# Kernel tuning notes

Measured on AMD Instinct MI355X. Metric: run time of the kernel, lower is better.

The kernel has to match this reference:

```python
import jax, jax.numpy as jnp
import numpy as np

N, IN, HID, H, OUT, G = 2048, 128, 128, 4, 10, 8
NEG_SLOPE = 0.2
THRESHOLD = 0.0


def setup_inputs() -> dict:
    key = jax.random.key(0)
    ks = jax.random.split(key, 18)
    s = 0.05
    return {
        "x": jax.random.normal(ks[0], (N, IN), jnp.float32),
        "attn_tensor": jax.random.normal(ks[1], (12, N, N), jnp.float32),
        "batch_idx": jnp.sort(jax.random.randint(ks[2], (N,), 0, G)),
        "conv_w": jax.random.normal(ks[3], (12,), jnp.float32) * s,
        "conv_b": jnp.zeros((), jnp.float32),
        "W1": jax.random.normal(ks[4], (IN, H * HID), jnp.float32) * s,
        "att_src1": jax.random.normal(ks[5], (H, HID), jnp.float32) * s,
        "att_dst1": jax.random.normal(ks[6], (H, HID), jnp.float32) * s,
        "att_edge1": jax.random.normal(ks[7], (H, HID), jnp.float32) * s,
        "We1": jax.random.normal(ks[8], (H * HID,), jnp.float32) * s,
        "b1": jnp.zeros((H * HID,), jnp.float32),
        "W2": jax.random.normal(ks[9], (H * HID, HID), jnp.float32) * s,
        "att_src2": jax.random.normal(ks[10], (1, HID), jnp.float32) * s,
        "att_dst2": jax.random.normal(ks[11], (1, HID), jnp.float32) * s,
        "att_edge2": jax.random.normal(ks[12], (1, HID), jnp.float32) * s,
        "We2": jax.random.normal(ks[13], (HID,), jnp.float32) * s,
        "b2": jnp.zeros((HID,), jnp.float32),
        "fc_w": jax.random.normal(ks[14], (HID, OUT), jnp.float32) * s,
        "fc_b": jnp.zeros((OUT,), jnp.float32),
    }


def gat_layer(x, adj, eattr, W, a_src, a_dst, a_edge, We, b, heads, out_ch):
    n = x.shape[0]
    h = (x @ W).reshape(n, heads, out_ch)            # [N,H,C]
    s_src = jnp.einsum('nhc,hc->nh', h, a_src)       # alpha contribution of source node
    s_dst = jnp.einsum('nhc,hc->nh', h, a_dst)       # alpha contribution of target node
    c_e = jnp.einsum('hc,hc->h', a_edge, We.reshape(heads, out_ch))  # scalar edge coeff per head
    # logits[s,t,h] for message s -> t (edge (s,t) means agg_mat[s,t] > thr)
    logits = s_src[:, None, :] + s_dst[None, :, :] + eattr[:, :, None] * c_e[None, None, :]
    logits = jnp.where(logits >= 0, logits, NEG_SLOPE * logits)  # leaky_relu(0.2)
    logits = jnp.where(adj[:, :, None], logits, -1e9)
    alpha = jax.nn.softmax(logits, axis=0)           # segment softmax over sources per target
    out = jnp.einsum('sth,shc->thc', alpha, h).reshape(n, heads * out_ch)
    return out + b


def reference(x, attn_tensor, batch_idx, conv_w, conv_b,
              W1, att_src1, att_dst1, att_edge1, We1, b1,
              W2, att_src2, att_dst2, att_edge2, We2, b2,
              fc_w, fc_b):
    # 1x1 conv over 12 attention channels -> dense [N,N] aggregated matrix
    agg = jnp.einsum('c,cst->st', conv_w, attn_tensor) + conv_b
    eye = jnp.eye(N, dtype=bool)
    mask_off = (agg > THRESHOLD) & (~eye)            # PyG GATConv removes then re-adds self loops
    # self-loop edge_attr = mean of incoming edge attrs per target (fill_value='mean')
    cnt = mask_off.sum(axis=0)
    mean_attr = jnp.where(mask_off, agg, 0.0).sum(axis=0) / jnp.maximum(cnt, 1)
    eattr = jnp.where(mask_off, agg, 0.0) + jnp.diag(mean_attr)
    adj = mask_off | eye

    h = gat_layer(x, adj, eattr, W1, att_src1, att_dst1, att_edge1, We1, b1, H, HID)
    h = jax.nn.relu(h)
    h = gat_layer(h, adj, eattr, W2, att_src2, att_dst2, att_edge2, We2, b2, 1, HID)

    sums = jax.ops.segment_sum(h, batch_idx, num_segments=G)
    counts = jax.ops.segment_sum(jnp.ones((N,), h.dtype), batch_idx, num_segments=G)
    pooled = sums / jnp.maximum(counts, 1.0)[:, None]  # global_mean_pool
    return jax.nn.log_softmax(pooled @ fc_w + fc_b, axis=1)
```

## Files before the change

### kernel.cpp

```cpp
#include <hip/hip_runtime.h>
#include <hip/hip_bf16.h>
#include <math.h>

#define NN 2048
#define NEG_SLOPE 0.2f

typedef __attribute__((ext_vector_type(8))) short bf16x8;
typedef __attribute__((ext_vector_type(4))) float f32x4;

static __device__ inline short f2bf(float x) {
  union { float f; unsigned u; } v;
  v.f = x;
  unsigned r = v.u + 0x7fffu + ((v.u >> 16) & 1u);
  return (short)(r >> 16);
}

static __device__ inline float bf2f(short b) {
  union { unsigned u; float f; } v;
  v.u = ((unsigned)(unsigned short)b) << 16;
  return v.f;
}

__global__ __launch_bounds__(256) void k_pre(
    const float* __restrict__ attn, const float* __restrict__ conv_w,
    const float* __restrict__ conv_b, const float* __restrict__ x,
    const float* __restrict__ W1, const float* __restrict__ W2,
    const float* __restrict__ asrc1, const float* __restrict__ adst1,
    const float* __restrict__ ae1, const float* __restrict__ We1,
    const float* __restrict__ ae2, const float* __restrict__ We2,
    __hip_bfloat16* __restrict__ aggTb, float* __restrict__ ssum_part,
    float* __restrict__ scnt_part, __hip_bfloat16* __restrict__ hTsw1,
    float* __restrict__ sspart1, float* __restrict__ sdpart1,
    __hip_bfloat16* __restrict__ w2t, float* __restrict__ ce) {
  const int b = blockIdx.x;
  const int tid = threadIdx.x;
  __shared__ __align__(16) char smem[34816];
  if (b < 512) {
    typedef short w1row[136];
    w1row* w1s = (w1row*)smem;
    const int mb = b >> 2, cblk = b & 3;
    const int m0 = mb * 16;
    for (int e = tid; e < 128 * 32; e += 256) {
      int k = e >> 5, cq = (e & 31) * 4;
      f32x4 v = *(const f32x4*)(W1 + (size_t)k * 512 + cblk * 128 + cq);
#pragma unroll
      for (int j = 0; j < 4; ++j) w1s[cq + j][k] = f2bf(v[j]);
    }
    __syncthreads();
    const int wv = tid >> 6;
    const int lane = tid & 63, row = lane & 15, kg = lane >> 4;
    const int nb = cblk * 4 + wv;
    const int n0l = wv * 32;
    const float* axrow = x + (size_t)(m0 + row) * 128 + kg * 8;
    f32x4 acc[2];
#pragma unroll
    for (int f = 0; f < 2; ++f) acc[f] = (f32x4){0.f, 0.f, 0.f, 0.f};
#pragma unroll
    for (int ks = 0; ks < 4; ++ks) {
      f32x4 xa = *(const f32x4*)(axrow + ks * 32);
      f32x4 xb = *(const f32x4*)(axrow + ks * 32 + 4);
      bf16x8 Af = {f2bf(xa[0]), f2bf(xa[1]), f2bf(xa[2]), f2bf(xa[3]),
                   f2bf(xb[0]), f2bf(xb[1]), f2bf(xb[2]), f2bf(xb[3])};
#pragma unroll
      for (int f = 0; f < 2; ++f) {
        bf16x8 Bf = *(const bf16x8*)&w1s[n0l + f * 16 + row][kg * 8 + ks * 32];
        acc[f] =
            __builtin_amdgcn_mfma_f32_16x16x32_bf16(Af, Bf, acc[f], 0, 0, 0);
      }
    }
    const int h = nb >> 2;
    float as[2], ad[2];
#pragma unroll
    for (int f = 0; f < 2; ++f) {
      int ch = (n0l + f * 16 + row) & 127;
      as[f] = asrc1[h * 128 + ch];
      ad[f] = adst1[h * 128 + ch];
    }
    float ps[4] = {0.f, 0.f, 0.f, 0.f}, pd[4] = {0.f, 0.f, 0.f, 0.f};
#pragma unroll
    for (int f = 0; f < 2; ++f)
#pragma unroll
      for (int r = 0; r < 4; ++r) {
        ps[r] += acc[f][r] * as[f];
        pd[r] += acc[f][r] * ad[f];
      }
#pragma unroll
    for (int m = 1; m < 16; m <<= 1) {
#pragma unroll
      for (int r = 0; r < 4; ++r) {
        ps[r] += __shfl_xor(ps[r], m);
        pd[r] += __shfl_xor(pd[r], m);
      }
    }
    if (row == 0) {
#pragma unroll
      for (int r = 0; r < 4; ++r) {
        int node = m0 + kg * 4 + r;
        sspart1[nb * NN + node] = ps[r];
        sdpart1[nb * NN + node] = pd[r];
      }
    }
#pragma unroll
    for (int f = 0; f < 2; ++f) {
      const int cbi = nb * 2 + f;
      short4 ct;
      ct.x = f2bf(acc[f][0]); ct.y = f2bf(acc[f][1]);
      ct.z = f2bf(acc[f][2]); ct.w = f2bf(acc[f][3]);
      size_t a4 =
          (size_t)cbi * (NN * 16) +
          (size_t)(((m0 >> 3) + (kg >> 1)) * 128 + row * 8 + (kg & 1) * 4);
      *(short4*)((short*)hTsw1 + a4) = ct;
    }
  } else if (b < 1536) {
    typedef float trow[68];
    trow* tile = (trow*)smem;
    const int b2 = b - 512;
    const int t0 = (b2 & 31) * 64;
    const int s0 = (b2 >> 5) * 64;
    const int sl = tid >> 4;
    const int t4 = (tid & 15) * 4;
    float w[12];
#pragma unroll
    for (int c = 0; c < 12; ++c) w[c] = conv_w[c];
    const float cb = conv_b[0];
    f32x4 acc[4];
#pragma unroll
    for (int k = 0; k < 4; ++k) acc[k] = (f32x4){cb, cb, cb, cb};
    for (int c = 0; c < 12; ++c) {
      const float* base =
          attn + (size_t)c * NN * NN + (size_t)(s0 + sl) * NN + t0 + t4;
#pragma unroll
      for (int k = 0; k < 4; ++k)
        acc[k] += w[c] * *(const f32x4*)(base + (size_t)k * 16 * NN);
    }
#pragma unroll
    for (int k = 0; k < 4; ++k) *(f32x4*)&tile[sl + 16 * k][t4] = acc[k];
    __syncthreads();
    const int tl = tid >> 2;
    const int sq = (tid & 3) * 16;
    const int tglob = t0 + tl;
    float psum = 0.f, pcnt = 0.f;
    short bb[16];
#pragma unroll
    for (int g = 0; g < 4; ++g) {
      f32x4 v = {tile[sq + 4 * g][tl], tile[sq + 4 * g + 1][tl],
                 tile[sq + 4 * g + 2][tl], tile[sq + 4 * g + 3][tl]};
#pragma unroll
      for (int j = 0; j < 4; ++j) {
        bb[4 * g + j] = f2bf(v[j]);
        int sglob = s0 + sq + 4 * g + j;
        bool m = (v[j] > 0.f) && (sglob != tglob);
        psum += m ? v[j] : 0.f;
        pcnt += m ? 1.f : 0.f;
      }
    }
    {
      short* orow = (short*)aggTb + (size_t)tglob * NN + s0 + sq;
      bf16x8 lo = {bb[0], bb[1], bb[2], bb[3], bb[4], bb[5], bb[6], bb[7]};
      bf16x8 hi = {bb[8], bb[9], bb[10], bb[11], bb[12], bb[13], bb[14], bb[15]};
      *(bf16x8*)orow = lo;
      *(bf16x8*)(orow + 8) = hi;
    }
    psum += __shfl_down(psum, 1); psum += __shfl_down(psum, 2);
    pcnt += __shfl_down(pcnt, 1); pcnt += __shfl_down(pcnt, 2);
    if ((tid & 3) == 0) {
      ssum_part[(b2 >> 5) * NN + tglob] = psum;
      scnt_part[(b2 >> 5) * NN + tglob] = pcnt;
    }
  } else if (b < 1568) {
#pragma unroll
    for (int k = 0; k < 8; ++k) {
      int o = (b - 1536) * 2048 + k * 256 + tid;
      ((short*)w2t)[o] = f2bf(W2[(o & 511) * 128 + (o >> 9)]);
    }
  } else {
    const int lane = tid & 63;
    const int wv = tid >> 6;
    float q1 = ae1[wv * 128 + lane] * We1[wv * 128 + lane] +
               ae1[wv * 128 + 64 + lane] * We1[wv * 128 + 64 + lane];
    for (int off = 32; off; off >>= 1) q1 += __shfl_down(q1, off);
    if (lane == 0) ce[wv] = q1;
    float q2 = ae2[lane] * We2[lane] + ae2[64 + lane] * We2[64 + lane];
    for (int off = 32; off; off >>= 1) q2 += __shfl_down(q2, off);
    if (tid == 0) ce[4] = q2;
  }
}

__global__ __launch_bounds__(256) void k_attn1(
    const __hip_bfloat16* __restrict__ aggTb,
    const __hip_bfloat16* __restrict__ hTsw1,
    const float* __restrict__ sspart1, const float* __restrict__ sdpart1,
    const float* __restrict__ ssum_part, const float* __restrict__ scnt_part,
    const float* __restrict__ ce_all, const float* __restrict__ b1,
    __hip_bfloat16* __restrict__ feat1b) {
  const int tid = threadIdx.x;
  const int t0 = (int)(blockIdx.x >> 2) * 16;
  const int h = (int)(blockIdx.x & 3u);
  __shared__ float ss_sh[2048];
  __shared__ float red[4][16][128];
  __shared__ float den_sh[4][16];
  __shared__ float mp_sh[2][16][16];
  __shared__ float ma_sh[16];
  for (int i = tid; i < 2048; i += 256)
    ss_sh[i] = sspart1[(4 * h + 0) * NN + i] + sspart1[(4 * h + 1) * NN + i] +
               sspart1[(4 * h + 2) * NN + i] + sspart1[(4 * h + 3) * NN + i];
  {
    int r = tid & 15, q2 = tid >> 4;
    float s_ = ssum_part[(size_t)(2 * q2) * NN + t0 + r] +
               ssum_part[(size_t)(2 * q2 + 1) * NN + t0 + r];
    float c_ = scnt_part[(size_t)(2 * q2) * NN + t0 + r] +
               scnt_part[(size_t)(2 * q2 + 1) * NN + t0 + r];
    mp_sh[0][q2][r] = s_;
    mp_sh[1][q2][r] = c_;
  }
  __syncthreads();
  if (tid < 16) {
    float s_ = 0.f, c_ = 0.f;
#pragma unroll
    for (int q = 0; q < 16; ++q) { s_ += mp_sh[0][q][tid]; c_ += mp_sh[1][q][tid]; }
    ma_sh[tid] = s_ / fmaxf(c_, 1.f);
  }
  __syncthreads();
  const int lane = tid & 63, w = tid >> 6, row = lane & 15, kg = lane >> 4;
  const int sbeg = w * 512;
  const int tRow = t0 + row;
  const float ma_t = ma_sh[row];
  const float ce = ce_all[h];
  const float sd_t = sdpart1[(4 * h + 0) * NN + tRow] +
                     sdpart1[(4 * h + 1) * NN + tRow] +
                     sdpart1[(4 * h + 2) * NN + tRow] +
                     sdpart1[(4 * h + 3) * NN + tRow];
  const short* arowb = (const short*)aggTb + (size_t)tRow * NN;
  const float* ssh = ss_sh + sbeg;
  const __hip_bfloat16* bbase =
      hTsw1 + (size_t)(h * 8) * (NN * 16) + kg * 128 + row * 8;
  f32x4 acc[8];
#pragma unroll
  for (int f = 0; f < 8; ++f) acc[f] = (f32x4){0.f, 0.f, 0.f, 0.f};
  float dpart = 0.f;
  for (int s0 = sbeg; s0 < sbeg + 512; s0 += 32) {
    const int sk = s0 + kg * 8;
    bf16x8 araw = *(const bf16x8*)(arowb + sk);
    f32x4 sv0 = *(const f32x4*)(ssh + (sk - sbeg));
    f32x4 sv1 = *(const f32x4*)(ssh + (sk - sbeg) + 4);
    float sv[8] = {sv0[0], sv0[1], sv0[2], sv0[3],
                   sv1[0], sv1[1], sv1[2], sv1[3]};
    short pb[8];
#pragma unroll
    for (int j = 0; j < 8; ++j) {
      const int s = sk + j;
      const float a = bf2f(araw[j]);
      const bool diag = (s == tRow);
      const float ev = diag ? ma_t : a;
      const bool adj = diag || (a > 0.f);
      float l = sv[j] + sd_t + ev * ce;
      l = fmaxf(l, NEG_SLOPE * l);
      const float p = adj ? __expf(l) : 0.f;
      dpart += p;
      pb[j] = f2bf(p);
    }
    bf16x8 A = {pb[0], pb[1], pb[2], pb[3], pb[4], pb[5], pb[6], pb[7]};
    const __hip_bfloat16* bp = bbase + (size_t)s0 * 16;
#pragma unroll
    for (int f = 0; f < 8; ++f) {
      bf16x8 B = *(const bf16x8*)(bp + (size_t)f * (NN * 16));
      acc[f] = __builtin_amdgcn_mfma_f32_16x16x32_bf16(A, B, acc[f], 0, 0, 0);
    }
  }
  dpart += __shfl_xor(dpart, 16);
  dpart += __shfl_xor(dpart, 32);
  __syncthreads();
#pragma unroll
  for (int f = 0; f < 8; ++f)
#pragma unroll
    for (int r = 0; r < 4; ++r) red[w][kg * 4 + r][f * 16 + row] = acc[f][r];
  if (lane < 16) den_sh[w][lane] = dpart;
  __syncthreads();
#pragma unroll
  for (int i = 0; i < 8; ++i) {
    int idx = i * 256 + tid;
    int t = idx >> 7, c = idx & 127;
    float nsum = red[0][t][c] + red[1][t][c] + red[2][t][c] + red[3][t][c];
    float dsum = den_sh[0][t] + den_sh[1][t] + den_sh[2][t] + den_sh[3][t];
    float v = nsum / dsum + b1[h * 128 + c];
    feat1b[(size_t)(t0 + t) * 512 + h * 128 + c] =
        __float2bfloat16(v > 0.f ? v : 0.f);
  }
}

__global__ __launch_bounds__(256) void k_gemm2(
    const __hip_bfloat16* __restrict__ feat1b,
    const __hip_bfloat16* __restrict__ w2t, const float* __restrict__ asrc2,
    const float* __restrict__ adst2, __hip_bfloat16* __restrict__ hTsw2,
    float* __restrict__ ssrc2, float* __restrict__ sdst2) {
  const int tid = threadIdx.x;
  const int wv = tid >> 6;
  const int w = (int)blockIdx.x * 4 + wv;
  const int lane = tid & 63, row = lane & 15, kg = lane >> 4;
  const int mb = w >> 2, nb = w & 3;
  const int m0 = mb * 16, n0 = nb * 32;
  __shared__ float sred[2][4][16];
  const __hip_bfloat16* arow = feat1b + (size_t)(m0 + row) * 512 + kg * 8;
  f32x4 acc[2];
#pragma unroll
  for (int f = 0; f < 2; ++f) acc[f] = (f32x4){0.f, 0.f, 0.f, 0.f};
#pragma unroll
  for (int ks = 0; ks < 16; ++ks) {
    bf16x8 Af = *(const bf16x8*)(arow + ks * 32);
#pragma unroll
    for (int f = 0; f < 2; ++f) {
      bf16x8 Bf = *(const bf16x8*)(w2t + (size_t)(n0 + f * 16 + row) * 512 +
                                   kg * 8 + ks * 32);
      acc[f] = __builtin_amdgcn_mfma_f32_16x16x32_bf16(Af, Bf, acc[f], 0, 0, 0);
    }
  }
  float as[2], ad[2];
#pragma unroll
  for (int f = 0; f < 2; ++f) {
    int ch = (n0 + f * 16 + row) & 127;
    as[f] = asrc2[ch];
    ad[f] = adst2[ch];
  }
  float ps[4] = {0.f, 0.f, 0.f, 0.f}, pd[4] = {0.f, 0.f, 0.f, 0.f};
#pragma unroll
  for (int f = 0; f < 2; ++f)
#pragma unroll
    for (int r = 0; r < 4; ++r) {
      ps[r] += acc[f][r] * as[f];
      pd[r] += acc[f][r] * ad[f];
    }
#pragma unroll
  for (int m = 1; m < 16; m <<= 1) {
#pragma unroll
    for (int r = 0; r < 4; ++r) {
      ps[r] += __shfl_xor(ps[r], m);
      pd[r] += __shfl_xor(pd[r], m);
    }
  }
  if (row == 0) {
#pragma unroll
    for (int r = 0; r < 4; ++r) {
      sred[0][wv][kg * 4 + r] = ps[r];
      sred[1][wv][kg * 4 + r] = pd[r];
    }
  }
  __syncthreads();
  if (tid < 16) {
    float s = sred[0][0][tid] + sred[0][1][tid] + sred[0][2][tid] +
              sred[0][3][tid];
    float d = sred[1][0][tid] + sred[1][1][tid] + sred[1][2][tid] +
              sred[1][3][tid];
    ssrc2[(int)blockIdx.x * 16 + tid] = s;
    sdst2[(int)blockIdx.x * 16 + tid] = d;
  }
#pragma unroll
  for (int f = 0; f < 2; ++f) {
    const int cbi = nb * 2 + f;
    short4 ct;
    ct.x = f2bf(acc[f][0]); ct.y = f2bf(acc[f][1]);
    ct.z = f2bf(acc[f][2]); ct.w = f2bf(acc[f][3]);
    size_t a4 = (size_t)cbi * (NN * 16) +
                (size_t)(((m0 >> 3) + (kg >> 1)) * 128 + row * 8 + (kg & 1) * 4);
    *(short4*)((short*)hTsw2 + a4) = ct;
  }
}

__global__ __launch_bounds__(256) void k_attn2(
    const __hip_bfloat16* __restrict__ aggTb,
    const __hip_bfloat16* __restrict__ hTsw2,
    const float* __restrict__ ssrc2, const float* __restrict__ sdst2,
    const float* __restrict__ ssum_part, const float* __restrict__ scnt_part,
    const float* __restrict__ ce_all, const float* __restrict__ b2,
    float* __restrict__ feat2) {
  const int tid = threadIdx.x;
  const int t0 = (int)(blockIdx.x >> 1) * 16;
  const int chalf = (int)(blockIdx.x & 1u);
  __shared__ float ss_sh[2048];
  __shared__ float red[4][16][64];
  __shared__ float den_sh[4][16];
  __shared__ float mp_sh[2][16][16];
  __shared__ float ma_sh[16];
  for (int i = tid; i < 2048; i += 256) ss_sh[i] = ssrc2[i];
  {
    int r = tid & 15, q2 = tid >> 4;
    float s_ = ssum_part[(size_t)(2 * q2) * NN + t0 + r] +
               ssum_part[(size_t)(2 * q2 + 1) * NN + t0 + r];
    float c_ = scnt_part[(size_t)(2 * q2) * NN + t0 + r] +
               scnt_part[(size_t)(2 * q2 + 1) * NN + t0 + r];
    mp_sh[0][q2][r] = s_;
    mp_sh[1][q2][r] = c_;
  }
  __syncthreads();
  if (tid < 16) {
    float s_ = 0.f, c_ = 0.f;
#pragma unroll
    for (int q = 0; q < 16; ++q) { s_ += mp_sh[0][q][tid]; c_ += mp_sh[1][q][tid]; }
    ma_sh[tid] = s_ / fmaxf(c_, 1.f);
  }
  __syncthreads();
  const int lane = tid & 63, w = tid >> 6, row = lane & 15, kg = lane >> 4;
  const int sbeg = w * 512;
  const int tRow = t0 + row;
  const float ma_t = ma_sh[row];
  const float ce = ce_all[4];
  const float sd_t = sdst2[tRow];
  const short* arowb = (const short*)aggTb + (size_t)tRow * NN;
  const float* ssh = ss_sh + sbeg;
  const __hip_bfloat16* bbase =
      hTsw2 + (size_t)(chalf * 4) * (NN * 16) + kg * 128 + row * 8;
  f32x4 acc[4];
#pragma unroll
  for (int f = 0; f < 4; ++f) acc[f] = (f32x4){0.f, 0.f, 0.f, 0.f};
  float dpart = 0.f;
  for (int s0 = sbeg; s0 < sbeg + 512; s0 += 32) {
    const int sk = s0 + kg * 8;
    bf16x8 araw = *(const bf16x8*)(arowb + sk);
    f32x4 sv0 = *(const f32x4*)(ssh + (sk - sbeg));
    f32x4 sv1 = *(const f32x4*)(ssh + (sk - sbeg) + 4);
    float sv[8] = {sv0[0], sv0[1], sv0[2], sv0[3],
                   sv1[0], sv1[1], sv1[2], sv1[3]};
    short pb[8];
#pragma unroll
    for (int j = 0; j < 8; ++j) {
      const int s = sk + j;
      const float a = bf2f(araw[j]);
      const bool diag = (s == tRow);
      const float ev = diag ? ma_t : a;
      const bool adj = diag || (a > 0.f);
      float l = sv[j] + sd_t + ev * ce;
      l = fmaxf(l, NEG_SLOPE * l);
      const float p = adj ? __expf(l) : 0.f;
      dpart += p;
      pb[j] = f2bf(p);
    }
    bf16x8 A = {pb[0], pb[1], pb[2], pb[3], pb[4], pb[5], pb[6], pb[7]};
    const __hip_bfloat16* bp = bbase + (size_t)s0 * 16;
#pragma unroll
    for (int f = 0; f < 4; ++f) {
      bf16x8 B = *(const bf16x8*)(bp + (size_t)f * (NN * 16));
      acc[f] = __builtin_amdgcn_mfma_f32_16x16x32_bf16(A, B, acc[f], 0, 0, 0);
    }
  }
  dpart += __shfl_xor(dpart, 16);
  dpart += __shfl_xor(dpart, 32);
  __syncthreads();
#pragma unroll
  for (int f = 0; f < 4; ++f)
#pragma unroll
    for (int r = 0; r < 4; ++r) red[w][kg * 4 + r][f * 16 + row] = acc[f][r];
  if (lane < 16) den_sh[w][lane] = dpart;
  __syncthreads();
#pragma unroll
  for (int i = 0; i < 4; ++i) {
    int idx = i * 256 + tid;
    int t = idx >> 6, c = idx & 63;
    float nsum = red[0][t][c] + red[1][t][c] + red[2][t][c] + red[3][t][c];
    float dsum = den_sh[0][t] + den_sh[1][t] + den_sh[2][t] + den_sh[3][t];
    feat2[(size_t)(t0 + t) * 128 + chalf * 64 + c] =
        nsum / dsum + b2[chalf * 64 + c];
  }
}

__global__ __launch_bounds__(256) void k_poolhead(
    const float* __restrict__ feat, const int* __restrict__ bidx,
    const float* __restrict__ fcw, const float* __restrict__ fcb,
    float* __restrict__ out) {
  const int g = blockIdx.x;
  const int tid = threadIdx.x;
  __shared__ int lo[2];
  __shared__ float ps2[256];
  __shared__ float lsh[10];
  if (tid == 0) { lo[0] = NN; lo[1] = NN; }
  __syncthreads();
  for (int n = tid; n < NN; n += 256) {
    int b = bidx[n];
    int bprev = (n == 0) ? -1 : bidx[n - 1];
    if (b >= g && bprev < g) atomicMin(&lo[0], n);
    if (b >= g + 1 && bprev < g + 1) atomicMin(&lo[1], n);
  }
  __syncthreads();
  int s = lo[0], e = lo[1];
  const int c = tid & 127, half = tid >> 7;
  float sum = 0.f;
  for (int n = s + half; n < e; n += 2) sum += feat[(size_t)n * 128 + c];
  ps2[tid] = sum;
  __syncthreads();
  if (tid < 128) {
    float cntf = (float)((e - s) > 1 ? (e - s) : 1);
    ps2[tid] = (ps2[tid] + ps2[tid + 128]) / cntf;
  }
  __syncthreads();
  if (tid < 10) {
    float v = fcb[tid];
    for (int ch = 0; ch < 128; ++ch) v += ps2[ch] * fcw[ch * 10 + tid];
    lsh[tid] = v;
  }
  __syncthreads();
  if (tid < 10) {
    float m = -1e30f;
    for (int i = 0; i < 10; ++i) m = fmaxf(m, lsh[i]);
    float den = 0.f;
    for (int i = 0; i < 10; ++i) den += expf(lsh[i] - m);
    out[g * 10 + tid] = lsh[tid] - m - logf(den);
  }
}

extern "C" void kernel_launch(void* const* d_in, const int* in_sizes, int n_in,
                              void* d_out, int out_size, void* d_ws,
                              size_t ws_size, hipStream_t stream) {
  (void)in_sizes; (void)n_in; (void)out_size; (void)ws_size;
  const float* x      = (const float*)d_in[0];
  const float* attn   = (const float*)d_in[1];
  const int*   bidx   = (const int*)d_in[2];
  const float* conv_w = (const float*)d_in[3];
  const float* conv_b = (const float*)d_in[4];
  const float* W1     = (const float*)d_in[5];
  const float* asrc1  = (const float*)d_in[6];
  const float* adst1  = (const float*)d_in[7];
  const float* aedge1 = (const float*)d_in[8];
  const float* We1    = (const float*)d_in[9];
  const float* b1     = (const float*)d_in[10];
  const float* W2     = (const float*)d_in[11];
  const float* asrc2  = (const float*)d_in[12];
  const float* adst2  = (const float*)d_in[13];
  const float* aedge2 = (const float*)d_in[14];
  const float* We2    = (const float*)d_in[15];
  const float* b2     = (const float*)d_in[16];
  const float* fcw    = (const float*)d_in[17];
  const float* fcb    = (const float*)d_in[18];

  float* ws = (float*)d_ws;
  __hip_bfloat16* aggTb = (__hip_bfloat16*)ws;
  float* feat2     = ws + 2097152;
  float* ssum_part = feat2 + 262144;
  float* scnt_part = ssum_part + 65536;
  float* sspart1   = scnt_part + 65536;
  float* sdpart1   = sspart1 + 32768;
  float* ssrc2     = sdpart1 + 32768;
  float* sdst2     = ssrc2 + 2048;
  float* ce        = sdst2 + 2048;
  float* bf        = ce + 64;
  __hip_bfloat16* w2t    = (__hip_bfloat16*)bf;
  __hip_bfloat16* hTsw1  = (__hip_bfloat16*)(bf + 32768);
  __hip_bfloat16* hTsw2  = (__hip_bfloat16*)(bf + 557056);
  __hip_bfloat16* feat1b = (__hip_bfloat16*)(bf + 688128);

  k_pre<<<1569, 256, 0, stream>>>(attn, conv_w, conv_b, x, W1, W2, asrc1,
                                  adst1, aedge1, We1, aedge2, We2, aggTb,
                                  ssum_part, scnt_part, hTsw1, sspart1,
                                  sdpart1, w2t, ce);
  k_attn1<<<512, 256, 0, stream>>>(aggTb, hTsw1, sspart1, sdpart1, ssum_part,
                                   scnt_part, ce, b1, feat1b);
  k_gemm2<<<128, 256, 0, stream>>>(feat1b, w2t, asrc2, adst2, hTsw2, ssrc2,
                                   sdst2);
  k_attn2<<<256, 256, 0, stream>>>(aggTb, hTsw2, ssrc2, sdst2, ssum_part,
                                   scnt_part, ce, b2, feat2);
  k_poolhead<<<8, 256, 0, stream>>>(feat2, bidx, fcw, fcb, (float*)d_out);
}
```

Before: 124.6 us.

## Split prep kernel, shrink conv tiles, and split attn2 over source halves

```diff
diff --git a/kernel.cpp b/kernel.cpp
--- a/kernel.cpp
+++ b/kernel.cpp
@@ -21,23 +21,75 @@
   return v.f;
 }
 
-__global__ __launch_bounds__(256) void k_pre(
+__global__ __launch_bounds__(256) void k_conv(
     const float* __restrict__ attn, const float* __restrict__ conv_w,
-    const float* __restrict__ conv_b, const float* __restrict__ x,
-    const float* __restrict__ W1, const float* __restrict__ W2,
-    const float* __restrict__ asrc1, const float* __restrict__ adst1,
-    const float* __restrict__ ae1, const float* __restrict__ We1,
-    const float* __restrict__ ae2, const float* __restrict__ We2,
-    __hip_bfloat16* __restrict__ aggTb, float* __restrict__ ssum_part,
-    float* __restrict__ scnt_part, __hip_bfloat16* __restrict__ hTsw1,
+    const float* __restrict__ conv_b, __hip_bfloat16* __restrict__ aggTb,
+    float* __restrict__ ssum_part, float* __restrict__ scnt_part) {
+  __shared__ float tile[32][68];
+  const int b = blockIdx.x;
+  const int tid = threadIdx.x;
+  const int t0 = (b & 31) * 64;
+  const int s0 = (b >> 5) * 32;
+  const int sl = tid >> 4;
+  const int t4 = (tid & 15) * 4;
+  float w[12];
+#pragma unroll
+  for (int c = 0; c < 12; ++c) w[c] = conv_w[c];
+  const float cb = conv_b[0];
+  f32x4 acc0 = {cb, cb, cb, cb}, acc1 = {cb, cb, cb, cb};
+#pragma unroll
+  for (int c = 0; c < 12; ++c) {
+    const float* base =
+        attn + (size_t)c * NN * NN + (size_t)(s0 + sl) * NN + t0 + t4;
+    acc0 += w[c] * *(const f32x4*)base;
+    acc1 += w[c] * *(const f32x4*)(base + (size_t)16 * NN);
+  }
+  *(f32x4*)&tile[sl][t4] = acc0;
+  *(f32x4*)&tile[sl + 16][t4] = acc1;
+  __syncthreads();
+  const int tl = tid >> 2;
+  const int sq = (tid & 3) * 8;
+  const int tglob = t0 + tl;
+  float psum = 0.f, pcnt = 0.f;
+  short bb[8];
+#pragma unroll
+  for (int g = 0; g < 2; ++g) {
+    f32x4 v = {tile[sq + 4 * g][tl], tile[sq + 4 * g + 1][tl],
+               tile[sq + 4 * g + 2][tl], tile[sq + 4 * g + 3][tl]};
+#pragma unroll
+    for (int j = 0; j < 4; ++j) {
+      bb[4 * g + j] = f2bf(v[j]);
+      int sglob = s0 + sq + 4 * g + j;
+      bool m = (v[j] > 0.f) && (sglob != tglob);
+      psum += m ? v[j] : 0.f;
+      pcnt += m ? 1.f : 0.f;
+    }
+  }
+  {
+    short* orow = (short*)aggTb + (size_t)tglob * NN + s0 + sq;
+    bf16x8 lo = {bb[0], bb[1], bb[2], bb[3], bb[4], bb[5], bb[6], bb[7]};
+    *(bf16x8*)orow = lo;
+  }
+  psum += __shfl_down(psum, 1); psum += __shfl_down(psum, 2);
+  pcnt += __shfl_down(pcnt, 1); pcnt += __shfl_down(pcnt, 2);
+  if ((tid & 3) == 0) {
+    ssum_part[(size_t)(b >> 5) * NN + tglob] = psum;
+    scnt_part[(size_t)(b >> 5) * NN + tglob] = pcnt;
+  }
+}
+
+__global__ __launch_bounds__(256) void k_aux(
+    const float* __restrict__ x, const float* __restrict__ W1,
+    const float* __restrict__ W2, const float* __restrict__ asrc1,
+    const float* __restrict__ adst1, const float* __restrict__ ae1,
+    const float* __restrict__ We1, const float* __restrict__ ae2,
+    const float* __restrict__ We2, __hip_bfloat16* __restrict__ hTsw1,
     float* __restrict__ sspart1, float* __restrict__ sdpart1,
     __hip_bfloat16* __restrict__ w2t, float* __restrict__ ce) {
   const int b = blockIdx.x;
   const int tid = threadIdx.x;
-  __shared__ __align__(16) char smem[34816];
   if (b < 512) {
-    typedef short w1row[136];
-    w1row* w1s = (w1row*)smem;
+    __shared__ short w1s[128][136];
     const int mb = b >> 2, cblk = b & 3;
     const int m0 = mb * 16;
     for (int e = tid; e < 128 * 32; e += 256) {
@@ -111,66 +163,10 @@
           (size_t)(((m0 >> 3) + (kg >> 1)) * 128 + row * 8 + (kg & 1) * 4);
       *(short4*)((short*)hTsw1 + a4) = ct;
     }
-  } else if (b < 1536) {
-    typedef float trow[68];
-    trow* tile = (trow*)smem;
-    const int b2 = b - 512;
-    const int t0 = (b2 & 31) * 64;
-    const int s0 = (b2 >> 5) * 64;
-    const int sl = tid >> 4;
-    const int t4 = (tid & 15) * 4;
-    float w[12];
-#pragma unroll
-    for (int c = 0; c < 12; ++c) w[c] = conv_w[c];
-    const float cb = conv_b[0];
-    f32x4 acc[4];
-#pragma unroll
-    for (int k = 0; k < 4; ++k) acc[k] = (f32x4){cb, cb, cb, cb};
-    for (int c = 0; c < 12; ++c) {
-      const float* base =
-          attn + (size_t)c * NN * NN + (size_t)(s0 + sl) * NN + t0 + t4;
-#pragma unroll
-      for (int k = 0; k < 4; ++k)
-        acc[k] += w[c] * *(const f32x4*)(base + (size_t)k * 16 * NN);
-    }
-#pragma unroll
-    for (int k = 0; k < 4; ++k) *(f32x4*)&tile[sl + 16 * k][t4] = acc[k];
-    __syncthreads();
-    const int tl = tid >> 2;
-    const int sq = (tid & 3) * 16;
-    const int tglob = t0 + tl;
-    float psum = 0.f, pcnt = 0.f;
-    short bb[16];
-#pragma unroll
-    for (int g = 0; g < 4; ++g) {
-      f32x4 v = {tile[sq + 4 * g][tl], tile[sq + 4 * g + 1][tl],
-                 tile[sq + 4 * g + 2][tl], tile[sq + 4 * g + 3][tl]};
-#pragma unroll
-      for (int j = 0; j < 4; ++j) {
-        bb[4 * g + j] = f2bf(v[j]);
-        int sglob = s0 + sq + 4 * g + j;
-        bool m = (v[j] > 0.f) && (sglob != tglob);
-        psum += m ? v[j] : 0.f;
-        pcnt += m ? 1.f : 0.f;
-      }
-    }
-    {
-      short* orow = (short*)aggTb + (size_t)tglob * NN + s0 + sq;
-      bf16x8 lo = {bb[0], bb[1], bb[2], bb[3], bb[4], bb[5], bb[6], bb[7]};
-      bf16x8 hi = {bb[8], bb[9], bb[10], bb[11], bb[12], bb[13], bb[14], bb[15]};
-      *(bf16x8*)orow = lo;
-      *(bf16x8*)(orow + 8) = hi;
-    }
-    psum += __shfl_down(psum, 1); psum += __shfl_down(psum, 2);
-    pcnt += __shfl_down(pcnt, 1); pcnt += __shfl_down(pcnt, 2);
-    if ((tid & 3) == 0) {
-      ssum_part[(b2 >> 5) * NN + tglob] = psum;
-      scnt_part[(b2 >> 5) * NN + tglob] = pcnt;
-    }
-  } else if (b < 1568) {
+  } else if (b < 544) {
 #pragma unroll
     for (int k = 0; k < 8; ++k) {
-      int o = (b - 1536) * 2048 + k * 256 + tid;
+      int o = (b - 512) * 2048 + k * 256 + tid;
       ((short*)w2t)[o] = f2bf(W2[(o & 511) * 128 + (o >> 9)]);
     }
   } else {
@@ -206,10 +202,12 @@
                sspart1[(4 * h + 2) * NN + i] + sspart1[(4 * h + 3) * NN + i];
   {
     int r = tid & 15, q2 = tid >> 4;
-    float s_ = ssum_part[(size_t)(2 * q2) * NN + t0 + r] +
-               ssum_part[(size_t)(2 * q2 + 1) * NN + t0 + r];
-    float c_ = scnt_part[(size_t)(2 * q2) * NN + t0 + r] +
-               scnt_part[(size_t)(2 * q2 + 1) * NN + t0 + r];
+    float s_ = 0.f, c_ = 0.f;
+#pragma unroll
+    for (int i = 0; i < 4; ++i) {
+      s_ += ssum_part[(size_t)(4 * q2 + i) * NN + t0 + r];
+      c_ += scnt_part[(size_t)(4 * q2 + i) * NN + t0 + r];
+    }
     mp_sh[0][q2][r] = s_;
     mp_sh[1][q2][r] = c_;
   }
@@ -370,23 +368,28 @@
     const __hip_bfloat16* __restrict__ hTsw2,
     const float* __restrict__ ssrc2, const float* __restrict__ sdst2,
     const float* __restrict__ ssum_part, const float* __restrict__ scnt_part,
-    const float* __restrict__ ce_all, const float* __restrict__ b2,
-    float* __restrict__ feat2) {
+    const float* __restrict__ ce_all, float* __restrict__ num2p,
+    float* __restrict__ den2p) {
   const int tid = threadIdx.x;
-  const int t0 = (int)(blockIdx.x >> 1) * 16;
-  const int chalf = (int)(blockIdx.x & 1u);
-  __shared__ float ss_sh[2048];
+  const int tt = (int)(blockIdx.x >> 2);
+  const int chalf = (int)((blockIdx.x >> 1) & 1u);
+  const int sh = (int)(blockIdx.x & 1u);
+  const int t0 = tt * 16;
+  const int soff = sh * 1024;
+  __shared__ float ss_sh[1024];
   __shared__ float red[4][16][64];
   __shared__ float den_sh[4][16];
   __shared__ float mp_sh[2][16][16];
   __shared__ float ma_sh[16];
-  for (int i = tid; i < 2048; i += 256) ss_sh[i] = ssrc2[i];
+  for (int i = tid; i < 1024; i += 256) ss_sh[i] = ssrc2[soff + i];
   {
     int r = tid & 15, q2 = tid >> 4;
-    float s_ = ssum_part[(size_t)(2 * q2) * NN + t0 + r] +
-               ssum_part[(size_t)(2 * q2 + 1) * NN + t0 + r];
-    float c_ = scnt_part[(size_t)(2 * q2) * NN + t0 + r] +
-               scnt_part[(size_t)(2 * q2 + 1) * NN + t0 + r];
+    float s_ = 0.f, c_ = 0.f;
+#pragma unroll
+    for (int i = 0; i < 4; ++i) {
+      s_ += ssum_part[(size_t)(4 * q2 + i) * NN + t0 + r];
+      c_ += scnt_part[(size_t)(4 * q2 + i) * NN + t0 + r];
+    }
     mp_sh[0][q2][r] = s_;
     mp_sh[1][q2][r] = c_;
   }
@@ -399,24 +402,23 @@
   }
   __syncthreads();
   const int lane = tid & 63, w = tid >> 6, row = lane & 15, kg = lane >> 4;
-  const int sbeg = w * 512;
+  const int sbeg = soff + w * 256;
   const int tRow = t0 + row;
   const float ma_t = ma_sh[row];
   const float ce = ce_all[4];
   const float sd_t = sdst2[tRow];
   const short* arowb = (const short*)aggTb + (size_t)tRow * NN;
-  const float* ssh = ss_sh + sbeg;
   const __hip_bfloat16* bbase =
       hTsw2 + (size_t)(chalf * 4) * (NN * 16) + kg * 128 + row * 8;
   f32x4 acc[4];
 #pragma unroll
   for (int f = 0; f < 4; ++f) acc[f] = (f32x4){0.f, 0.f, 0.f, 0.f};
   float dpart = 0.f;
-  for (int s0 = sbeg; s0 < sbeg + 512; s0 += 32) {
+  for (int s0 = sbeg; s0 < sbeg + 256; s0 += 32) {
     const int sk = s0 + kg * 8;
     bf16x8 araw = *(const bf16x8*)(arowb + sk);
-    f32x4 sv0 = *(const f32x4*)(ssh + (sk - sbeg));
-    f32x4 sv1 = *(const f32x4*)(ssh + (sk - sbeg) + 4);
+    f32x4 sv0 = *(const f32x4*)(ss_sh + (sk - soff));
+    f32x4 sv1 = *(const f32x4*)(ss_sh + (sk - soff) + 4);
     float sv[8] = {sv0[0], sv0[1], sv0[2], sv0[3],
                    sv1[0], sv1[1], sv1[2], sv1[3]};
     short pb[8];
@@ -455,14 +457,17 @@
     int idx = i * 256 + tid;
     int t = idx >> 6, c = idx & 63;
     float nsum = red[0][t][c] + red[1][t][c] + red[2][t][c] + red[3][t][c];
-    float dsum = den_sh[0][t] + den_sh[1][t] + den_sh[2][t] + den_sh[3][t];
-    feat2[(size_t)(t0 + t) * 128 + chalf * 64 + c] =
-        nsum / dsum + b2[chalf * 64 + c];
+    num2p[((size_t)sh * NN + t0 + t) * 128 + chalf * 64 + c] = nsum;
+  }
+  if (chalf == 0 && tid < 16) {
+    float d = den_sh[0][tid] + den_sh[1][tid] + den_sh[2][tid] + den_sh[3][tid];
+    den2p[(size_t)sh * NN + t0 + tid] = d;
   }
 }
 
 __global__ __launch_bounds__(256) void k_poolhead(
-    const float* __restrict__ feat, const int* __restrict__ bidx,
+    const float* __restrict__ num2p, const float* __restrict__ den2p,
+    const int* __restrict__ bidx, const float* __restrict__ b2,
     const float* __restrict__ fcw, const float* __restrict__ fcb,
     float* __restrict__ out) {
   const int g = blockIdx.x;
@@ -482,12 +487,17 @@
   int s = lo[0], e = lo[1];
   const int c = tid & 127, half = tid >> 7;
   float sum = 0.f;
-  for (int n = s + half; n < e; n += 2) sum += feat[(size_t)n * 128 + c];
+  for (int n = s + half; n < e; n += 2) {
+    float nsum = num2p[(size_t)n * 128 + c] +
+                 num2p[((size_t)NN + n) * 128 + c];
+    float dsum = den2p[n] + den2p[NN + n];
+    sum += nsum / dsum;
+  }
   ps2[tid] = sum;
   __syncthreads();
   if (tid < 128) {
     float cntf = (float)((e - s) > 1 ? (e - s) : 1);
-    ps2[tid] = (ps2[tid] + ps2[tid + 128]) / cntf;
+    ps2[tid] = (ps2[tid] + ps2[tid + 128]) / cntf + b2[tid];
   }
   __syncthreads();
   if (tid < 10) {
@@ -531,29 +541,31 @@
 
   float* ws = (float*)d_ws;
   __hip_bfloat16* aggTb = (__hip_bfloat16*)ws;
-  float* feat2     = ws + 2097152;
-  float* ssum_part = feat2 + 262144;
-  float* scnt_part = ssum_part + 65536;
-  float* sspart1   = scnt_part + 65536;
+  float* ssum_part = ws + 2097152;
+  float* scnt_part = ssum_part + 131072;
+  float* sspart1   = scnt_part + 131072;
   float* sdpart1   = sspart1 + 32768;
   float* ssrc2     = sdpart1 + 32768;
   float* sdst2     = ssrc2 + 2048;
-  float* ce        = sdst2 + 2048;
+  float* num2p     = sdst2 + 2048;
+  float* den2p     = num2p + 524288;
+  float* ce        = den2p + 4096;
   float* bf        = ce + 64;
   __hip_bfloat16* w2t    = (__hip_bfloat16*)bf;
   __hip_bfloat16* hTsw1  = (__hip_bfloat16*)(bf + 32768);
   __hip_bfloat16* hTsw2  = (__hip_bfloat16*)(bf + 557056);
   __hip_bfloat16* feat1b = (__hip_bfloat16*)(bf + 688128);
 
-  k_pre<<<1569, 256, 0, stream>>>(attn, conv_w, conv_b, x, W1, W2, asrc1,
-                                  adst1, aedge1, We1, aedge2, We2, aggTb,
-                                  ssum_part, scnt_part, hTsw1, sspart1,
-                                  sdpart1, w2t, ce);
+  k_conv<<<2048, 256, 0, stream>>>(attn, conv_w, conv_b, aggTb, ssum_part,
+                                   scnt_part);
+  k_aux<<<545, 256, 0, stream>>>(x, W1, W2, asrc1, adst1, aedge1, We1, aedge2,
+                                 We2, hTsw1, sspart1, sdpart1, w2t, ce);
   k_attn1<<<512, 256, 0, stream>>>(aggTb, hTsw1, sspart1, sdpart1, ssum_part,
                                    scnt_part, ce, b1, feat1b);
   k_gemm2<<<128, 256, 0, stream>>>(feat1b, w2t, asrc2, adst2, hTsw2, ssrc2,
                                    sdst2);
-  k_attn2<<<256, 256, 0, stream>>>(aggTb, hTsw2, ssrc2, sdst2, ssum_part,
-                                   scnt_part, ce, b2, feat2);
-  k_poolhead<<<8, 256, 0, stream>>>(feat2, bidx, fcw, fcb, (float*)d_out);
-}
+  k_attn2<<<512, 256, 0, stream>>>(aggTb, hTsw2, ssrc2, sdst2, ssum_part,
+                                   scnt_part, ce, num2p, den2p);
+  k_poolhead<<<8, 256, 0, stream>>>(num2p, den2p, bidx, b2, fcw, fcb,
+                                    (float*)d_out);
+}
```

After: 147.0 us. +18.0%, slower.
